# Optimization experiments

Hardware: AMD Instinct MI355X
Metric: run time of the kernel (lower is better)

Reference implementation:

```python
import jax, jax.numpy as jnp
import numpy as np

B, S, E = 4, 2048, 1024
H, D = 16, 64  # attention_dim * num_heads == E


def setup_inputs() -> dict:
    key = jax.random.key(0)
    ks = jax.random.split(key, 7)
    scale = 1.0 / np.sqrt(E)
    return {
        "x": jax.random.normal(ks[0], (B, S, E), dtype=jnp.float32),
        "mask": jnp.ones((B, S), dtype=jnp.int32),
        "Wq": jax.random.normal(ks[1], (E, H * D), dtype=jnp.float32) * scale,
        "bq": jnp.zeros((H * D,), dtype=jnp.float32),
        "Wk": jax.random.normal(ks[2], (E, H * D), dtype=jnp.float32) * scale,
        "bk": jnp.zeros((H * D,), dtype=jnp.float32),
        "Wv": jax.random.normal(ks[3], (E, H * D), dtype=jnp.float32) * scale,
        "bv": jnp.zeros((H * D,), dtype=jnp.float32),
    }


def reference(x, mask, Wq, bq, Wk, bk, Wv, bv):
    b, s, _ = x.shape
    # projections -> [B, S, H*D] -> [B, H, S, D]
    def split_heads(t):
        return t.reshape(b, s, H, D).transpose(0, 2, 1, 3)

    q = split_heads(x @ Wq + bq)
    k = split_heads(x @ Wk + bk)
    v = split_heads(x @ Wv + bv)

    # full [B, H, S, S] attention scores (non-fused, as in the original)
    scores = jnp.einsum("bhsd,bhtd->bhst", q, k) / jnp.sqrt(jnp.asarray(D, x.dtype))
    # key-padding mask [B, S] -> [B, 1, 1, S]; masked_fill(mask == 0, -inf)
    m = mask[:, None, None, :]
    scores = jnp.where(m == 0, jnp.asarray(-jnp.inf, scores.dtype), scores)
    weights = jax.nn.softmax(scores, axis=-1)
    y = jnp.einsum("bhst,bhtd->bhsd", weights, v)
    # [B, H, S, D] -> [B, S, H*D]
    return y.transpose(0, 2, 1, 3).reshape(b, s, H * D)
```

## Files before the change

### kernel.cpp

```cpp
#include <hip/hip_runtime.h>
#include <hip/hip_bf16.h>
#include <stdint.h>

typedef unsigned short u16;
typedef __attribute__((ext_vector_type(8))) short bf16x8;
typedef __attribute__((ext_vector_type(4))) float f32x4;
typedef __attribute__((ext_vector_type(16))) float f32x16;

#define DEVI static __device__ __forceinline__

constexpr int Bc = 4, Sc = 2048, Hc = 16;

DEVI u16 f2bf(float f) {
  __hip_bfloat16 h = __float2bfloat16(f);
  u16 u; __builtin_memcpy(&u, &h, 2);
  return u;
}

DEVI uint32_t pk2(float a, float b) {
  float2 f2; f2.x = a; f2.y = b;
  __hip_bfloat162 h = __float22bfloat162_rn(f2);
  uint32_t r; __builtin_memcpy(&r, &h, 4);
  return r;
}

DEVI void gl_lds16(const void* g, void* l) {
  __builtin_amdgcn_global_load_lds(
      (__attribute__((address_space(1))) void*)(uintptr_t)g,
      (__attribute__((address_space(3))) void*)l, 16, 0, 0);
}

__global__ __launch_bounds__(256) void cast_x_kernel(const float* __restrict__ x,
                                                     u16* __restrict__ xb, int n4) {
  int i = blockIdx.x * 256 + threadIdx.x;
  if (i >= n4) return;
  float4 a = reinterpret_cast<const float4*>(x)[i];
  uint2 r;
  r.x = (uint32_t)f2bf(a.x) | ((uint32_t)f2bf(a.y) << 16);
  r.y = (uint32_t)f2bf(a.z) | ((uint32_t)f2bf(a.w) << 16);
  reinterpret_cast<uint2*>(xb)[i] = r;
}

__global__ __launch_bounds__(256) void cast_wt_kernel(const float* __restrict__ Wq,
                                                      const float* __restrict__ Wk,
                                                      const float* __restrict__ Wv,
                                                      u16* __restrict__ wt) {
  __shared__ float ls[64][66];
  int blk = blockIdx.x;
  int t = blk >> 8, rem = blk & 255;
  int kb = rem >> 4, nb = rem & 15;
  const float* W = (t == 0) ? Wq : (t == 1) ? Wk : Wv;
  int tid = threadIdx.x;
#pragma unroll
  for (int i = 0; i < 16; ++i) {
    int idx = tid + i * 256;
    int r = idx >> 6, c = idx & 63;
    ls[r][c] = W[(size_t)(kb * 64 + r) * 1024 + nb * 64 + c];
  }
  __syncthreads();
  u16* wto = wt + (size_t)t * 1024 * 1024;
#pragma unroll
  for (int i = 0; i < 16; ++i) {
    int idx = tid + i * 256;
    int n = idx >> 6, k = idx & 63;
    wto[(size_t)(nb * 64 + n) * 1024 + kb * 64 + k] = f2bf(ls[k][n]);
  }
}

__global__ __launch_bounds__(256) void qkv_gemm_kernel(const u16* __restrict__ xb,
                                                       const u16* __restrict__ wt,
                                                       const float* __restrict__ bq,
                                                       const float* __restrict__ bk,
                                                       const float* __restrict__ bv,
                                                       u16* __restrict__ qb,
                                                       u16* __restrict__ kbuf,
                                                       u16* __restrict__ vtb) {
  __shared__ __align__(16) u16 Ab[128][64];
  __shared__ __align__(16) u16 Bb[128][64];
  int tile = blockIdx.x;
  int tn = tile % 24, tm = tile / 24;
  int m0 = tm * 128, n0 = tn * 128;
  int tid = threadIdx.x;
  int w = tid >> 6, lane = tid & 63;
  int wr = w >> 1, wc = w & 1;
  f32x4 acc[4][4] = {};
  int arow = wr * 64 + (lane & 15);
  int brow = wc * 64 + (lane & 15);
  int kfrag = (lane >> 4) * 8;
  for (int kt = 0; kt < 16; ++kt) {
    int k0 = kt * 64;
#pragma unroll
    for (int i = 0; i < 4; ++i) {
      int r = 32 * w + 8 * i + (lane >> 3);
      gl_lds16(xb + (size_t)(m0 + r) * 1024 + k0 + (lane & 7) * 8, &Ab[32 * w + 8 * i][0]);
      gl_lds16(wt + (size_t)(n0 + r) * 1024 + k0 + (lane & 7) * 8, &Bb[32 * w + 8 * i][0]);
    }
    __syncthreads();
#pragma unroll
    for (int kk = 0; kk < 2; ++kk) {
      bf16x8 af[4], bfr[4];
#pragma unroll
      for (int mi = 0; mi < 4; ++mi)
        af[mi] = *(const bf16x8*)&Ab[arow + mi * 16][kk * 32 + kfrag];
#pragma unroll
      for (int ni = 0; ni < 4; ++ni)
        bfr[ni] = *(const bf16x8*)&Bb[brow + ni * 16][kk * 32 + kfrag];
#pragma unroll
      for (int mi = 0; mi < 4; ++mi)
#pragma unroll
        for (int ni = 0; ni < 4; ++ni)
          acc[mi][ni] = __builtin_amdgcn_mfma_f32_16x16x32_bf16(af[mi], bfr[ni], acc[mi][ni], 0, 0, 0);
    }
    __syncthreads();
  }
  int tsel = n0 >> 10;
  int nl0 = n0 & 1023;
  const float* bias = (tsel == 0) ? bq : (tsel == 1) ? bk : bv;
  float scale = (tsel == 0) ? 0.18033688011112042f : 1.0f;
  if (tsel == 2) {
#pragma unroll
    for (int ni = 0; ni < 4; ++ni) {
      int ncol = nl0 + wc * 64 + ni * 16 + (lane & 15);
      float bia = bias[ncol];
      int h = ncol >> 6, d = ncol & 63;
#pragma unroll
      for (int mi = 0; mi < 4; ++mi) {
#pragma unroll
        for (int jj = 0; jj < 4; ++jj) {
          int m = m0 + wr * 64 + mi * 16 + (lane >> 4) * 4 + jj;
          int b = m >> 11, s = m & 2047;
          int ks = (s & ~12) | ((s & 4) << 1) | ((s & 8) >> 1);
          vtb[(((size_t)(b * Hc + h) * 64 + d) << 11) + ks] = f2bf(acc[mi][ni][jj] + bia);
        }
      }
    }
  } else {
    u16* outp = (tsel == 0) ? qb : kbuf;
#pragma unroll
    for (int ni = 0; ni < 4; ++ni) {
      int ncol = nl0 + wc * 64 + ni * 16 + (lane & 15);
      float bia = bias[ncol];
      int h = ncol >> 6, d = ncol & 63;
#pragma unroll
      for (int mi = 0; mi < 4; ++mi) {
#pragma unroll
        for (int jj = 0; jj < 4; ++jj) {
          int m = m0 + wr * 64 + mi * 16 + (lane >> 4) * 4 + jj;
          int b = m >> 11, s = m & 2047;
          outp[(((size_t)(b * Hc + h) * Sc + s) << 6) + d] = f2bf((acc[mi][ni][jj] + bia) * scale);
        }
      }
    }
  }
}

__global__ __launch_bounds__(256) void attn_kernel(const u16* __restrict__ qb,
                                                   const u16* __restrict__ kbuf,
                                                   const u16* __restrict__ vtb,
                                                   const int* __restrict__ mask,
                                                   float* __restrict__ out) {
  __shared__ __align__(16) char kvlds[2][2][8192];
  __shared__ uint32_t mbits[64];
  int bid = blockIdx.x;
  int bh = bid & 63, qblk = bid >> 6;
  int b = bh >> 4, h = bh & 15;
  int tid = threadIdx.x, lane = tid & 63;
  int w = tid >> 6;
  int col = lane & 31, hi = lane >> 5;
  int qw = qblk * 128 + w * 32;
  const u16* Qp = qb + (size_t)bh * Sc * 64;
  const char* KpB = (const char*)(kbuf + (size_t)bh * Sc * 64);
  const char* VpB = (const char*)(vtb + (size_t)bh * 64 * Sc);

  if (tid < 64) {
    const int* mp = mask + b * Sc + tid * 32;
    uint32_t mv = 0;
#pragma unroll
    for (int i = 0; i < 32; ++i) mv |= (mp[i] ? 1u : 0u) << i;
    mbits[tid] = mv;
  }

  bf16x8 qf[4];
#pragma unroll
  for (int dc = 0; dc < 4; ++dc)
    qf[dc] = *(const bf16x8*)(Qp + (size_t)(qw + col) * 64 + dc * 16 + hi * 8);
  __syncthreads();

  int skey = tid >> 3, sseg = tid & 7;
  int sx = (sseg ^ (skey & 7)) << 4;
  const char* ksrc0 = KpB + (size_t)skey * 128 + sx;
  const char* ksrc1 = ksrc0 + 32 * 128;
  const char* vsrc0 = VpB + (size_t)skey * (Sc * 2) + sx;
  const char* vsrc1 = vsrc0 + (size_t)32 * (Sc * 2);
  int dst0 = tid * 16, dst1 = tid * 16 + 4096;

#define STAGE(t)                                             \
  {                                                          \
    char* kb_ = kvlds[(t) & 1][0];                           \
    char* vb_ = kvlds[(t) & 1][1];                           \
    size_t ko_ = (size_t)(t) * 8192;                         \
    size_t vo_ = (size_t)(t) * 128;                          \
    gl_lds16(ksrc0 + ko_, kb_ + dst0);                       \
    gl_lds16(ksrc1 + ko_, kb_ + dst1);                       \
    gl_lds16(vsrc0 + vo_, vb_ + dst0);                       \
    gl_lds16(vsrc1 + vo_, vb_ + dst1);                       \
  }

  STAGE(0);

  f32x16 yacc0 = {}, yacc1 = {};
  float m = -1e30f, l = 0.f;
  int kx = (hi << 4) ^ ((col & 7) << 4);
  int colb = col * 128;

  for (int t = 0; t < 32; ++t) {
    if (t < 31) {
      STAGE(t + 1);
      asm volatile("s_waitcnt vmcnt(4)" ::: "memory");
    } else {
      asm volatile("s_waitcnt vmcnt(0)" ::: "memory");
    }
    __builtin_amdgcn_s_barrier();
    __builtin_amdgcn_sched_barrier(0);
    const char* Kb = kvlds[t & 1][0];
    const char* Vb = kvlds[t & 1][1];
    bf16x8 kf0[4], kf1[4], vfa[4], vfb[4];
#pragma unroll
    for (int dc = 0; dc < 4; ++dc) {
      kf0[dc] = *(const bf16x8*)(Kb + colb + ((dc << 5) ^ kx));
      kf1[dc] = *(const bf16x8*)(Kb + colb + 4096 + ((dc << 5) ^ kx));
    }
#pragma unroll
    for (int kc = 0; kc < 2; ++kc)
#pragma unroll
      for (int dn = 0; dn < 2; ++dn) {
        vfa[kc * 2 + dn] = *(const bf16x8*)(Vb + colb + dn * 4096 + ((kc << 5) ^ kx));
        vfb[kc * 2 + dn] =
            *(const bf16x8*)(Vb + colb + dn * 4096 + (64 ^ (kc << 5) ^ kx));
      }
    f32x16 s0 = {}, s1 = {};
    __builtin_amdgcn_s_setprio(1);
#pragma unroll
    for (int dc = 0; dc < 4; ++dc)
      s0 = __builtin_amdgcn_mfma_f32_32x32x16_bf16(kf0[dc], qf[dc], s0, 0, 0, 0);
#pragma unroll
    for (int dc = 0; dc < 4; ++dc)
      s1 = __builtin_amdgcn_mfma_f32_32x32x16_bf16(kf1[dc], qf[dc], s1, 0, 0, 0);
    __builtin_amdgcn_s_setprio(0);

    uint32_t mw0 = mbits[2 * t], mw1 = mbits[2 * t + 1];
    if (mw0 != 0xffffffffu || mw1 != 0xffffffffu) {
#pragma unroll
      for (int r = 0; r < 16; ++r) {
        int bi = (r & 3) + 8 * (r >> 2) + 4 * hi;
        s0[r] += ((mw0 >> bi) & 1) ? 0.f : -1e30f;
        s1[r] += ((mw1 >> bi) & 1) ? 0.f : -1e30f;
      }
    }
    float tm0 = fmaxf(fmaxf(fmaxf(s0[0], s0[1]), fmaxf(s0[2], s0[3])),
                      fmaxf(fmaxf(s0[4], s0[5]), fmaxf(s0[6], s0[7])));
    float tm1 = fmaxf(fmaxf(fmaxf(s0[8], s0[9]), fmaxf(s0[10], s0[11])),
                      fmaxf(fmaxf(s0[12], s0[13]), fmaxf(s0[14], s0[15])));
    float tm2 = fmaxf(fmaxf(fmaxf(s1[0], s1[1]), fmaxf(s1[2], s1[3])),
                      fmaxf(fmaxf(s1[4], s1[5]), fmaxf(s1[6], s1[7])));
    float tm3 = fmaxf(fmaxf(fmaxf(s1[8], s1[9]), fmaxf(s1[10], s1[11])),
                      fmaxf(fmaxf(s1[12], s1[13]), fmaxf(s1[14], s1[15])));
    float tmax = fmaxf(fmaxf(tm0, tm1), fmaxf(tm2, tm3));
    tmax = fmaxf(tmax, __shfl_xor(tmax, 32));
    if (!__all(tmax <= m + 8.0f)) {
      float mnew = fmaxf(m, tmax);
      float alpha = __builtin_amdgcn_exp2f(m - mnew);
      m = mnew;
      l *= alpha;
#pragma unroll
      for (int r = 0; r < 16; ++r) {
        float ar = __shfl(alpha, (r & 3) + 8 * (r >> 2) + 4 * hi);
        yacc0[r] *= ar;
        yacc1[r] *= ar;
      }
    }
    float lsum = 0.f;
#pragma unroll
    for (int r = 0; r < 16; ++r) {
      s0[r] = __builtin_amdgcn_exp2f(s0[r] - m);
      lsum += s0[r];
    }
#pragma unroll
    for (int r = 0; r < 16; ++r) {
      s1[r] = __builtin_amdgcn_exp2f(s1[r] - m);
      lsum += s1[r];
    }
    lsum += __shfl_xor(lsum, 32);
    l += lsum;

    {
      uint32_t pw[8];
#pragma unroll
      for (int i = 0; i < 8; ++i) pw[i] = pk2(s0[2 * i], s0[2 * i + 1]);
      bf16x8 pa0, pa1;
      __builtin_memcpy(&pa0, &pw[0], 16);
      __builtin_memcpy(&pa1, &pw[4], 16);
      __builtin_amdgcn_s_setprio(1);
      yacc0 = __builtin_amdgcn_mfma_f32_32x32x16_bf16(pa0, vfa[0], yacc0, 0, 0, 0);
      yacc1 = __builtin_amdgcn_mfma_f32_32x32x16_bf16(pa0, vfa[1], yacc1, 0, 0, 0);
      yacc0 = __builtin_amdgcn_mfma_f32_32x32x16_bf16(pa1, vfa[2], yacc0, 0, 0, 0);
      yacc1 = __builtin_amdgcn_mfma_f32_32x32x16_bf16(pa1, vfa[3], yacc1, 0, 0, 0);
      __builtin_amdgcn_s_setprio(0);
    }
    {
      uint32_t pw[8];
#pragma unroll
      for (int i = 0; i < 8; ++i) pw[i] = pk2(s1[2 * i], s1[2 * i + 1]);
      bf16x8 pa0, pa1;
      __builtin_memcpy(&pa0, &pw[0], 16);
      __builtin_memcpy(&pa1, &pw[4], 16);
      __builtin_amdgcn_s_setprio(1);
      yacc0 = __builtin_amdgcn_mfma_f32_32x32x16_bf16(pa0, vfb[0], yacc0, 0, 0, 0);
      yacc1 = __builtin_amdgcn_mfma_f32_32x32x16_bf16(pa0, vfb[1], yacc1, 0, 0, 0);
      yacc0 = __builtin_amdgcn_mfma_f32_32x32x16_bf16(pa1, vfb[2], yacc0, 0, 0, 0);
      yacc1 = __builtin_amdgcn_mfma_f32_32x32x16_bf16(pa1, vfb[3], yacc1, 0, 0, 0);
      __builtin_amdgcn_s_setprio(0);
    }
    __builtin_amdgcn_sched_barrier(0);
    __builtin_amdgcn_s_barrier();
  }

  float linv = 1.0f / l;
#pragma unroll
  for (int r = 0; r < 16; ++r) {
    int rq = (r & 3) + 8 * (r >> 2) + 4 * hi;
    float rl = __shfl(linv, rq);
    size_t o = ((size_t)(b * Sc + qw + rq) << 10) + h * 64;
    out[o + col] = yacc0[r] * rl;
    out[o + 32 + col] = yacc1[r] * rl;
  }
#undef STAGE
}

extern "C" void kernel_launch(void* const* d_in, const int* in_sizes, int n_in,
                              void* d_out, int out_size, void* d_ws, size_t ws_size,
                              hipStream_t stream) {
  const float* x  = (const float*)d_in[0];
  const int* mask = (const int*)d_in[1];
  const float* Wq = (const float*)d_in[2];
  const float* bq = (const float*)d_in[3];
  const float* Wk = (const float*)d_in[4];
  const float* bk = (const float*)d_in[5];
  const float* Wv = (const float*)d_in[6];
  const float* bv = (const float*)d_in[7];
  float* out = (float*)d_out;

  char* ws = (char*)d_ws;
  const size_t SZ_XB = (size_t)8192 * 1024 * 2;
  const size_t SZ_WT = (size_t)3 * 1024 * 1024 * 2;
  const size_t SZ_T  = (size_t)8192 * 1024 * 2;
  u16* xb  = (u16*)ws;
  u16* wt  = (u16*)(ws + SZ_XB);
  u16* qb  = (u16*)(ws + SZ_XB + SZ_WT);
  u16* kb  = (u16*)(ws + SZ_XB + SZ_WT + SZ_T);
  u16* vtb = (u16*)(ws + SZ_XB + SZ_WT + 2 * SZ_T);

  cast_x_kernel<<<8192, 256, 0, stream>>>(x, xb, 8192 * 1024 / 4);
  cast_wt_kernel<<<768, 256, 0, stream>>>(Wq, Wk, Wv, wt);
  qkv_gemm_kernel<<<1536, 256, 0, stream>>>(xb, wt, bq, bk, bv, qb, kb, vtb);
  attn_kernel<<<1024, 256, 0, stream>>>(qb, kb, vtb, mask, out);
}
```

Before: 216.7 us.

## Restructure QKV GEMM with 256x128 tiles, double-buffered LDS and swizzle

The QKV projection GEMM now runs 512-thread blocks on 256x128 output tiles. It double-buffers the K stages in 96KB of XOR-swizzled LDS, prefetching two stages ahead with explicit vmcnt waits. The MFMA work is split into four phases with barriers and setprio, and block IDs are remapped so neighbouring blocks share tiles for L2 reuse. The aim is to hide global-load latency, avoid LDS bank conflicts and raise GEMM throughput, at the cost of higher LDS use per block and more complex synchronisation.

```diff
diff --git a/kernel.cpp b/kernel.cpp
--- a/kernel.cpp
+++ b/kernel.cpp
@@ -67,7 +67,7 @@
   }
 }
 
-__global__ __launch_bounds__(256) void qkv_gemm_kernel(const u16* __restrict__ xb,
+__global__ __launch_bounds__(512) void qkv_gemm_kernel(const u16* __restrict__ xb,
                                                        const u16* __restrict__ wt,
                                                        const float* __restrict__ bq,
                                                        const float* __restrict__ bk,
@@ -75,44 +75,128 @@
                                                        u16* __restrict__ qb,
                                                        u16* __restrict__ kbuf,
                                                        u16* __restrict__ vtb) {
-  __shared__ __align__(16) u16 Ab[128][64];
-  __shared__ __align__(16) u16 Bb[128][64];
-  int tile = blockIdx.x;
-  int tn = tile % 24, tm = tile / 24;
-  int m0 = tm * 128, n0 = tn * 128;
+  __shared__ __align__(16) char glds[98304];
+  int bid = blockIdx.x;
+  int sw = (bid & 7) * 96 + (bid >> 3);
+  int tm = sw & 31, tn = sw >> 5;
+  int m0 = tm * 256, n0 = tn * 128;
   int tid = threadIdx.x;
   int w = tid >> 6, lane = tid & 63;
-  int wr = w >> 1, wc = w & 1;
+  int wm = w >> 1, wn = w & 1;
+
+  int srow = tid >> 3, sseg = tid & 7;
+  int sx = (sseg ^ (srow & 7)) << 4;
+  const char* Asrc = (const char*)xb + (size_t)(m0 + srow) * 2048 + sx;
+  const char* Bsrc = (const char*)wt + (size_t)(n0 + srow) * 2048 + sx;
+  int sdst = tid * 16;
+
+#define GSTAGE(t)                                                  \
+  {                                                                \
+    char* ab_ = glds + ((t) & 1) * 32768;                          \
+    char* bb_ = glds + 65536 + ((t) & 1) * 16384;                  \
+    size_t ko_ = (size_t)(t) * 128;                                \
+    gl_lds16(Asrc + ko_, ab_ + sdst);                              \
+    gl_lds16(Asrc + 64 * 2048 + ko_, ab_ + 8192 + sdst);           \
+    gl_lds16(Asrc + 128 * 2048 + ko_, ab_ + 16384 + sdst);         \
+    gl_lds16(Asrc + 192 * 2048 + ko_, ab_ + 24576 + sdst);         \
+    gl_lds16(Bsrc + ko_, bb_ + sdst);                              \
+    gl_lds16(Bsrc + 64 * 2048 + ko_, bb_ + 8192 + sdst);           \
+  }
+
+  GSTAGE(0);
+  GSTAGE(1);
+
   f32x4 acc[4][4] = {};
-  int arow = wr * 64 + (lane & 15);
-  int brow = wc * 64 + (lane & 15);
-  int kfrag = (lane >> 4) * 8;
-  for (int kt = 0; kt < 16; ++kt) {
-    int k0 = kt * 64;
-#pragma unroll
-    for (int i = 0; i < 4; ++i) {
-      int r = 32 * w + 8 * i + (lane >> 3);
-      gl_lds16(xb + (size_t)(m0 + r) * 1024 + k0 + (lane & 7) * 8, &Ab[32 * w + 8 * i][0]);
-      gl_lds16(wt + (size_t)(n0 + r) * 1024 + k0 + (lane & 7) * 8, &Bb[32 * w + 8 * i][0]);
-    }
-    __syncthreads();
-#pragma unroll
-    for (int kk = 0; kk < 2; ++kk) {
-      bf16x8 af[4], bfr[4];
-#pragma unroll
-      for (int mi = 0; mi < 4; ++mi)
-        af[mi] = *(const bf16x8*)&Ab[arow + mi * 16][kk * 32 + kfrag];
-#pragma unroll
-      for (int ni = 0; ni < 4; ++ni)
-        bfr[ni] = *(const bf16x8*)&Bb[brow + ni * 16][kk * 32 + kfrag];
-#pragma unroll
-      for (int mi = 0; mi < 4; ++mi)
-#pragma unroll
-        for (int ni = 0; ni < 4; ++ni)
-          acc[mi][ni] = __builtin_amdgcn_mfma_f32_16x16x32_bf16(af[mi], bfr[ni], acc[mi][ni], 0, 0, 0);
-    }
-    __syncthreads();
-  }
+  int rA = (wm & 1) * 64 + (lane & 15);
+  int rB = wn * 64 + (lane & 15);
+  int kq = (lane >> 4) << 4;
+  int axk = ((rA & 7) << 4);
+  int bxk = ((rB & 7) << 4);
+
+  for (int t = 0; t < 16; ++t) {
+    const char* Ab = glds + (t & 1) * 32768 + (wm >> 1) * 16384;
+    const char* Bb = glds + 65536 + (t & 1) * 16384;
+    if (t < 15) {
+      asm volatile("s_waitcnt vmcnt(6)" ::: "memory");
+    } else {
+      asm volatile("s_waitcnt vmcnt(0)" ::: "memory");
+    }
+    __builtin_amdgcn_s_barrier();
+    __builtin_amdgcn_sched_barrier(0);
+
+    bf16x8 af01[2][2], af23[2][2], bf[4][2];
+#pragma unroll
+    for (int mi = 0; mi < 2; ++mi)
+#pragma unroll
+      for (int kk = 0; kk < 2; ++kk)
+        af01[mi][kk] = *(const bf16x8*)(Ab + (rA + mi * 16) * 128 + ((kk * 64 + kq) ^ axk));
+#pragma unroll
+    for (int ni = 0; ni < 2; ++ni)
+#pragma unroll
+      for (int kk = 0; kk < 2; ++kk)
+        bf[ni][kk] = *(const bf16x8*)(Bb + (rB + ni * 16) * 128 + ((kk * 64 + kq) ^ bxk));
+    __builtin_amdgcn_s_setprio(1);
+#pragma unroll
+    for (int kk = 0; kk < 2; ++kk)
+#pragma unroll
+      for (int mi = 0; mi < 2; ++mi)
+#pragma unroll
+        for (int ni = 0; ni < 2; ++ni)
+          acc[mi][ni] = __builtin_amdgcn_mfma_f32_16x16x32_bf16(af01[mi][kk], bf[ni][kk],
+                                                                acc[mi][ni], 0, 0, 0);
+    __builtin_amdgcn_s_setprio(0);
+    __builtin_amdgcn_s_barrier();
+
+#pragma unroll
+    for (int ni = 2; ni < 4; ++ni)
+#pragma unroll
+      for (int kk = 0; kk < 2; ++kk)
+        bf[ni][kk] = *(const bf16x8*)(Bb + (rB + ni * 16) * 128 + ((kk * 64 + kq) ^ bxk));
+    __builtin_amdgcn_s_setprio(1);
+#pragma unroll
+    for (int kk = 0; kk < 2; ++kk)
+#pragma unroll
+      for (int mi = 0; mi < 2; ++mi)
+#pragma unroll
+        for (int ni = 2; ni < 4; ++ni)
+          acc[mi][ni] = __builtin_amdgcn_mfma_f32_16x16x32_bf16(af01[mi][kk], bf[ni][kk],
+                                                                acc[mi][ni], 0, 0, 0);
+    __builtin_amdgcn_s_setprio(0);
+    __builtin_amdgcn_s_barrier();
+
+#pragma unroll
+    for (int mi = 0; mi < 2; ++mi)
+#pragma unroll
+      for (int kk = 0; kk < 2; ++kk)
+        af23[mi][kk] =
+            *(const bf16x8*)(Ab + (rA + (mi + 2) * 16) * 128 + ((kk * 64 + kq) ^ axk));
+    __builtin_amdgcn_s_setprio(1);
+#pragma unroll
+    for (int kk = 0; kk < 2; ++kk)
+#pragma unroll
+      for (int mi = 0; mi < 2; ++mi)
+#pragma unroll
+        for (int ni = 2; ni < 4; ++ni)
+          acc[mi + 2][ni] = __builtin_amdgcn_mfma_f32_16x16x32_bf16(af23[mi][kk], bf[ni][kk],
+                                                                    acc[mi + 2][ni], 0, 0, 0);
+    __builtin_amdgcn_s_setprio(0);
+    __builtin_amdgcn_s_barrier();
+
+    if (t < 14) GSTAGE(t + 2);
+    __builtin_amdgcn_s_setprio(1);
+#pragma unroll
+    for (int kk = 0; kk < 2; ++kk)
+#pragma unroll
+      for (int mi = 0; mi < 2; ++mi)
+#pragma unroll
+        for (int ni = 0; ni < 2; ++ni)
+          acc[mi + 2][ni] = __builtin_amdgcn_mfma_f32_16x16x32_bf16(af23[mi][kk], bf[ni][kk],
+                                                                    acc[mi + 2][ni], 0, 0, 0);
+    __builtin_amdgcn_s_setprio(0);
+    __builtin_amdgcn_s_barrier();
+  }
+#undef GSTAGE
+
   int tsel = n0 >> 10;
   int nl0 = n0 & 1023;
   const float* bias = (tsel == 0) ? bq : (tsel == 1) ? bk : bv;
@@ -120,14 +204,14 @@
   if (tsel == 2) {
 #pragma unroll
     for (int ni = 0; ni < 4; ++ni) {
-      int ncol = nl0 + wc * 64 + ni * 16 + (lane & 15);
+      int ncol = nl0 + wn * 64 + ni * 16 + (lane & 15);
       float bia = bias[ncol];
       int h = ncol >> 6, d = ncol & 63;
 #pragma unroll
       for (int mi = 0; mi < 4; ++mi) {
 #pragma unroll
         for (int jj = 0; jj < 4; ++jj) {
-          int m = m0 + wr * 64 + mi * 16 + (lane >> 4) * 4 + jj;
+          int m = m0 + wm * 64 + mi * 16 + (lane >> 4) * 4 + jj;
           int b = m >> 11, s = m & 2047;
           int ks = (s & ~12) | ((s & 4) << 1) | ((s & 8) >> 1);
           vtb[(((size_t)(b * Hc + h) * 64 + d) << 11) + ks] = f2bf(acc[mi][ni][jj] + bia);
@@ -138,14 +222,14 @@
     u16* outp = (tsel == 0) ? qb : kbuf;
 #pragma unroll
     for (int ni = 0; ni < 4; ++ni) {
-      int ncol = nl0 + wc * 64 + ni * 16 + (lane & 15);
+      int ncol = nl0 + wn * 64 + ni * 16 + (lane & 15);
       float bia = bias[ncol];
       int h = ncol >> 6, d = ncol & 63;
 #pragma unroll
       for (int mi = 0; mi < 4; ++mi) {
 #pragma unroll
         for (int jj = 0; jj < 4; ++jj) {
-          int m = m0 + wr * 64 + mi * 16 + (lane >> 4) * 4 + jj;
+          int m = m0 + wm * 64 + mi * 16 + (lane >> 4) * 4 + jj;
           int b = m >> 11, s = m & 2047;
           outp[(((size_t)(b * Hc + h) * Sc + s) << 6) + d] = f2bf((acc[mi][ni][jj] + bia) * scale);
         }
@@ -362,6 +446,6 @@
 
   cast_x_kernel<<<8192, 256, 0, stream>>>(x, xb, 8192 * 1024 / 4);
   cast_wt_kernel<<<768, 256, 0, stream>>>(Wq, Wk, Wv, wt);
-  qkv_gemm_kernel<<<1536, 256, 0, stream>>>(xb, wt, bq, bk, bv, qb, kb, vtb);
+  qkv_gemm_kernel<<<768, 512, 0, stream>>>(xb, wt, bq, bk, bv, qb, kb, vtb);
   attn_kernel<<<1024, 256, 0, stream>>>(qb, kb, vtb, mask, out);
 }
```

Result: no change. 215.6 us (-0.5%).
